# Kernel tuning notes

Hardware: AMD Instinct MI355X
Metric: run time of the kernel (lower is better)

## Reference

```python
import jax, jax.numpy as jnp
import numpy as np

N = 8192
D = 128
NUM_CLASSES = 100
EPS = 1e-8  # torch CosineSimilarity default eps


def _l2_normalize(x):
    # torch cosine sim divides by max(||x||, eps)
    n = jnp.sqrt(jnp.sum(x * x, axis=-1, keepdims=True))
    return x / jnp.maximum(n, EPS)


def _remove_diag(M):
    # [n, n] -> [n, n-1], dropping the diagonal, no boolean gather needed
    n = M.shape[0]
    return M.reshape(-1)[1:].reshape(n - 1, n + 1)[:, :-1].reshape(n, n - 1)


def setup_inputs() -> dict:
    key = jax.random.key(0)
    k1, k2, k3, k4 = jax.random.split(key, 4)
    inst_embed = jax.random.normal(k1, (N, D), dtype=jnp.float32)
    proxy = jax.random.normal(k2, (N, D), dtype=jnp.float32)
    negative_mask = jax.random.randint(k3, (NUM_CLASSES, N), 0, 2).astype(jnp.float32)
    labels = jax.random.randint(k4, (N,), 0, NUM_CLASSES, dtype=jnp.int64) if jax.config.jax_enable_x64 else jax.random.randint(k4, (N,), 0, NUM_CLASSES, dtype=jnp.int32)
    return {
        "inst_embed": inst_embed,
        "proxy": proxy,
        "negative_mask": negative_mask,
        "labels": labels,
        "temperature": jnp.float32(0.07),
        "margin": jnp.float32(0.0),
    }


def reference(inst_embed, proxy, negative_mask, labels, temperature, margin):
    xn = _l2_normalize(inst_embed)                       # [N, D]
    # pairwise cosine similarity via normalize + matmul (not NxNxD broadcast)
    sim = xn @ xn.T                                      # [N, N]
    instance_zone = jnp.exp((_remove_diag(sim) - margin) / temperature)  # [N, N-1]

    pn = _l2_normalize(proxy)
    inst2proxy_positive = jnp.exp((jnp.sum(xn * pn, axis=-1) - margin) / temperature)  # [N]

    # pos_collected_numerator == True branch
    mask = _remove_diag(negative_mask[labels])           # [N, N-1]
    numerator = jnp.sum(instance_zone * mask, axis=1) + inst2proxy_positive
    denominator = inst2proxy_positive + jnp.sum(instance_zone, axis=1)
    return -jnp.mean(jnp.log(numerator / denominator))
```

## Files before the change

### kernel.cpp

```cpp
#include <hip/hip_runtime.h>
#include <stdint.h>

#define NROWS 8192
#define DD 128
#define EPS 1e-8f
#define LOG2E 1.4426950408889634f

#define SPLIT 16
#define RPB 256
#define CPT 32
#define LDS_COL 272
#define NT ((NROWS / SPLIT) / CPT)
#define NORM_BLOCKS (NROWS / 4)
#define PACK_BLOCKS 3200

typedef __bf16 bf16x8 __attribute__((ext_vector_type(8)));
typedef float f32x4 __attribute__((ext_vector_type(4)));

__device__ __forceinline__ unsigned int f2bf(float f) {
  union { float f; unsigned int u; } v; v.f = f;
  unsigned int u = v.u;
  return (u + 0x7fffu + ((u >> 16) & 1u)) >> 16;
}
__device__ __forceinline__ float bf2f(unsigned int b) {
  union { unsigned int u; float f; } v; v.u = b << 16;
  return v.f;
}

__global__ __launch_bounds__(256) void norm_kernel(
    const float* __restrict__ x, const float* __restrict__ pr,
    const float* __restrict__ nm, const int* __restrict__ lb,
    const float* __restrict__ tptr,
    unsigned short* __restrict__ xnA, unsigned short* __restrict__ xnB,
    float* __restrict__ p, float* __restrict__ eself, float* __restrict__ mii,
    float* __restrict__ tot, float* __restrict__ msk,
    unsigned int* __restrict__ packed, float* __restrict__ out)
{
  int wave = threadIdx.x >> 6, lane = threadIdx.x & 63;
  int bx = blockIdx.x;

  if (bx >= NORM_BLOCKS) {
    int widx = (bx - NORM_BLOCKS) * 4 + wave;
    int cls = widx >> 7;
    int w64 = widx & 127;
    float v = nm[(size_t)cls * NROWS + w64 * 64 + lane];
    unsigned long long b = __ballot(v != 0.0f);
    if (lane == 0) {
      packed[cls * 256 + w64 * 2] = (unsigned int)b;
      packed[cls * 256 + w64 * 2 + 1] = (unsigned int)(b >> 32);
    }
    return;
  }

  int row = bx * 4 + wave;
  float2 xv = ((const float2*)(x + (size_t)row * DD))[lane];
  float2 pv = ((const float2*)(pr + (size_t)row * DD))[lane];
  float sx = xv.x * xv.x + xv.y * xv.y;
  float sp = pv.x * pv.x + pv.y * pv.y;
  float dp = xv.x * pv.x + xv.y * pv.y;
  #pragma unroll
  for (int m = 1; m < 64; m <<= 1) {
    sx += __shfl_xor(sx, m);
    sp += __shfl_xor(sp, m);
    dp += __shfl_xor(dp, m);
  }
  float inx = 1.f / fmaxf(sqrtf(sx), EPS);
  float inp = 1.f / fmaxf(sqrtf(sp), EPS);
  float s1 = LOG2E / tptr[0];

  unsigned int a0 = f2bf(xv.x * inx * s1), a1 = f2bf(xv.y * inx * s1);
  unsigned int b0 = f2bf(xv.x * inx),      b1 = f2bf(xv.y * inx);
  ((unsigned int*)(xnA + (size_t)row * DD))[lane] = a0 | (a1 << 16);
  ((unsigned int*)(xnB + (size_t)row * DD))[lane] = b0 | (b1 << 16);

  float ss = bf2f(a0) * bf2f(b0) + bf2f(a1) * bf2f(b1);
  #pragma unroll
  for (int m = 1; m < 64; m <<= 1) ss += __shfl_xor(ss, m);

  if (lane == 0) {
    p[row] = __builtin_amdgcn_exp2f(dp * inx * inp * s1);
    eself[row] = __builtin_amdgcn_exp2f(ss);
    mii[row] = nm[(size_t)lb[row] * NROWS + row];
    tot[row] = 0.f;
    msk[row] = 0.f;
    if (row == 0) out[0] = 0.f;
  }
}

__global__ __launch_bounds__(256, 2) void main_kernel(
    const unsigned short* __restrict__ xnA_u, const unsigned short* __restrict__ xnB_u,
    const unsigned int* __restrict__ packed, const int* __restrict__ labels,
    float* __restrict__ tot, float* __restrict__ msk)
{
  __shared__ unsigned char lds[2][CPT * LDS_COL];
  int tid = threadIdx.x;
  int wave = tid >> 6, lane = tid & 63;
  int q = lane >> 4, c = lane & 15;
  int rbase = blockIdx.x * RPB + wave * 16;

  const bf16x8* xnvA = (const bf16x8*)xnA_u;

  bf16x8 a[4][4];
  #pragma unroll
  for (int st = 0; st < 4; st++) {
    const bf16x8* b = xnvA + (size_t)(rbase + st * 64 + c) * (DD / 8) + q;
    a[st][0] = b[0]; a[st][1] = b[4]; a[st][2] = b[8]; a[st][3] = b[12];
  }

  int jb = blockIdx.y * (NROWS / SPLIT);

  unsigned int offP[4][4];
  #pragma unroll
  for (int st = 0; st < 4; st++) {
    #pragma unroll
    for (int k = 0; k < 4; k++) {
      offP[st][k] = (unsigned int)labels[rbase + st * 64 + q * 4 + k] * 256u
                  + (unsigned int)(jb >> 5);
    }
  }
  float tacc[4][4], macc[4][4];
  #pragma unroll
  for (int st = 0; st < 4; st++)
    #pragma unroll
    for (int k = 0; k < 4; k++) { tacc[st][k] = 0.f; macc[st][k] = 0.f; }

  int scol = tid >> 4, schunk = tid & 15;
  const char* gB = (const char*)xnB_u;
  const char* gbase = gB + (size_t)(jb + scol) * 256 + schunk * 16;
  unsigned int ldsoff = (unsigned int)(scol * LDS_COL + schunk * 16);

  uint4 g0 = *(const uint4*)(gbase);
  uint4 g1 = *(const uint4*)(gbase + 16 * 256);
  unsigned int wn[4][4];
  #pragma unroll
  for (int st = 0; st < 4; st++)
    #pragma unroll
    for (int k = 0; k < 4; k++) wn[st][k] = packed[offP[st][k]];
  *(uint4*)(lds[0] + ldsoff)                = g0;
  *(uint4*)(lds[0] + ldsoff + 16 * LDS_COL) = g1;
  __syncthreads();

  for (int t = 0; t < NT; t++) {
    unsigned int wc[4][4];
    #pragma unroll
    for (int st = 0; st < 4; st++)
      #pragma unroll
      for (int k = 0; k < 4; k++) wc[st][k] = wn[st][k];

    if (t + 1 < NT) {
      const char* gb = gbase + (size_t)(t + 1) * (CPT * 256);
      g0 = *(const uint4*)(gb);
      g1 = *(const uint4*)(gb + 16 * 256);
      #pragma unroll
      for (int st = 0; st < 4; st++)
        #pragma unroll
        for (int k = 0; k < 4; k++) wn[st][k] = packed[offP[st][k] + t + 1];
    }

    const unsigned char* buf = lds[t & 1];
    #pragma unroll
    for (int s = 0; s < 2; s++) {
      const bf16x8* bl = (const bf16x8*)(buf + (unsigned)(s * 16 + c) * LDS_COL + q * 16);
      bf16x8 b0 = bl[0], b1 = bl[4], b2 = bl[8], b3 = bl[12];

      f32x4 acc[4];
      #pragma unroll
      for (int st = 0; st < 4; st++) acc[st] = (f32x4){0, 0, 0, 0};
      #pragma unroll
      for (int st = 0; st < 4; st++)
        acc[st] = __builtin_amdgcn_mfma_f32_16x16x32_bf16(a[st][0], b0, acc[st], 0, 0, 0);
      #pragma unroll
      for (int st = 0; st < 4; st++)
        acc[st] = __builtin_amdgcn_mfma_f32_16x16x32_bf16(a[st][1], b1, acc[st], 0, 0, 0);
      #pragma unroll
      for (int st = 0; st < 4; st++)
        acc[st] = __builtin_amdgcn_mfma_f32_16x16x32_bf16(a[st][2], b2, acc[st], 0, 0, 0);
      #pragma unroll
      for (int st = 0; st < 4; st++)
        acc[st] = __builtin_amdgcn_mfma_f32_16x16x32_bf16(a[st][3], b3, acc[st], 0, 0, 0);

      int pos = s * 16 + c;
      #pragma unroll
      for (int st = 0; st < 4; st++) {
        #pragma unroll
        for (int k = 0; k < 4; k++) {
          float e = __builtin_amdgcn_exp2f(acc[st][k]);
          tacc[st][k] += e;
          int sm;
          asm("v_bfe_i32 %0, %1, %2, 1" : "=v"(sm) : "v"(wc[st][k]), "v"(pos));
          union { float f; int i; } u;
          u.f = e; u.i &= sm;
          macc[st][k] += u.f;
        }
      }
    }

    if (t + 1 < NT) {
      unsigned char* nb = (unsigned char*)lds[(t + 1) & 1];
      *(uint4*)(nb + ldsoff)                = g0;
      *(uint4*)(nb + ldsoff + 16 * LDS_COL) = g1;
    }
    __syncthreads();
  }

  #pragma unroll
  for (int sh = 1; sh < 16; sh <<= 1) {
    #pragma unroll
    for (int st = 0; st < 4; st++) {
      #pragma unroll
      for (int k = 0; k < 4; k++) {
        tacc[st][k] += __shfl_xor(tacc[st][k], sh);
        macc[st][k] += __shfl_xor(macc[st][k], sh);
      }
    }
  }
  if (c == 0) {
    #pragma unroll
    for (int st = 0; st < 4; st++) {
      #pragma unroll
      for (int k = 0; k < 4; k++) {
        int r = rbase + st * 64 + q * 4 + k;
        atomicAdd(&tot[r], tacc[st][k]);
        atomicAdd(&msk[r], macc[st][k]);
      }
    }
  }
}

__global__ __launch_bounds__(256) void loss_kernel(
    const float* __restrict__ p, const float* __restrict__ tot,
    const float* __restrict__ msk, const float* __restrict__ eself,
    const float* __restrict__ mii, float* __restrict__ out)
{
  __shared__ float sd[4];
  int r = blockIdx.x * 256 + threadIdx.x;
  float pi = p[r];
  float es = eself[r];
  float t = tot[r] - es;
  float m = msk[r] - es * mii[r];
  float v = __builtin_amdgcn_logf(pi + t) - __builtin_amdgcn_logf(pi + m);
  float s = v * (1.0f / (LOG2E * (float)NROWS));
  #pragma unroll
  for (int sh = 1; sh < 64; sh <<= 1) s += __shfl_xor(s, sh);
  int wave = threadIdx.x >> 6, lane = threadIdx.x & 63;
  if (lane == 0) sd[wave] = s;
  __syncthreads();
  if (threadIdx.x == 0) atomicAdd(out, sd[0] + sd[1] + sd[2] + sd[3]);
}

extern "C" void kernel_launch(void* const* d_in, const int* in_sizes, int n_in,
                              void* d_out, int out_size, void* d_ws, size_t ws_size,
                              hipStream_t stream) {
  const float* x  = (const float*)d_in[0];
  const float* pr = (const float*)d_in[1];
  const float* nm = (const float*)d_in[2];
  const int*   lb = (const int*)d_in[3];
  const float* tp = (const float*)d_in[4];

  char* ws = (char*)d_ws;
  unsigned short* xnA = (unsigned short*)ws;
  unsigned short* xnB = xnA + (size_t)NROWS * DD;
  float* p     = (float*)(xnB + (size_t)NROWS * DD);
  float* tot   = p + NROWS;
  float* msk   = tot + NROWS;
  float* eself = msk + NROWS;
  float* miiv  = eself + NROWS;
  unsigned int* packed = (unsigned int*)(miiv + NROWS);
  float* out = (float*)d_out;

  norm_kernel<<<NORM_BLOCKS + PACK_BLOCKS, 256, 0, stream>>>(
      x, pr, nm, lb, tp, xnA, xnB, p, eself, miiv, tot, msk, packed, out);
  main_kernel<<<dim3(NROWS / RPB, SPLIT), 256, 0, stream>>>(xnA, xnB, packed,
                                                            lb, tot, msk);
  loss_kernel<<<NROWS / 256, 256, 0, stream>>>(p, tot, msk, eself, miiv, out);
}
```

Before: 106.5 us.

## Exploit Gram-matrix symmetry with upper-triangular 128x128 tile pairs

Replaces the split-column streaming loop with one block per upper-triangular 128x128 tile pair. Each block computes sim once and accumulates both row sums and column sums, masking the column contribution with the transposed label mask bits. This roughly halves the MFMA and exp work. In exchange it adds a second mask extraction per element, more atomics, and drops the in-block double-buffered pipelining, since each block now holds only one tile.

```diff
diff --git a/kernel.cpp b/kernel.cpp
--- a/kernel.cpp
+++ b/kernel.cpp
@@ -6,11 +6,10 @@
 #define EPS 1e-8f
 #define LOG2E 1.4426950408889634f
 
-#define SPLIT 16
-#define RPB 256
-#define CPT 32
+#define TB 128
+#define NTILE (NROWS / TB)
+#define NPAIRS (NTILE * (NTILE + 1) / 2)
 #define LDS_COL 272
-#define NT ((NROWS / SPLIT) / CPT)
 #define NORM_BLOCKS (NROWS / 4)
 #define PACK_BLOCKS 3200
 
@@ -92,115 +91,115 @@
     const unsigned int* __restrict__ packed, const int* __restrict__ labels,
     float* __restrict__ tot, float* __restrict__ msk)
 {
-  __shared__ unsigned char lds[2][CPT * LDS_COL];
+  __shared__ unsigned char lds[TB * LDS_COL];
   int tid = threadIdx.x;
   int wave = tid >> 6, lane = tid & 63;
   int q = lane >> 4, c = lane & 15;
-  int rbase = blockIdx.x * RPB + wave * 16;
+  int wm = wave >> 1, wn = wave & 1;
+
+  int bid = blockIdx.x;
+  int ri = (int)((129.0f - sqrtf(129.0f * 129.0f - 8.0f * (float)bid)) * 0.5f);
+  while (ri * (129 - ri) / 2 > bid) ri--;
+  while ((ri + 1) * (128 - ri) / 2 <= bid) ri++;
+  int cj = ri + (bid - ri * (129 - ri) / 2);
+  int rblock = ri * TB, colbase = cj * TB;
+
+  int scol = tid & 127, sh8 = (tid >> 7) * 8;
+  const uint4* gsrc = (const uint4*)((const char*)xnB_u + (size_t)(colbase + scol) * 256) + sh8;
+  uint4 stg[8];
+  #pragma unroll
+  for (int u = 0; u < 8; u++) stg[u] = gsrc[u];
 
   const bf16x8* xnvA = (const bf16x8*)xnA_u;
-
   bf16x8 a[4][4];
   #pragma unroll
   for (int st = 0; st < 4; st++) {
-    const bf16x8* b = xnvA + (size_t)(rbase + st * 64 + c) * (DD / 8) + q;
-    a[st][0] = b[0]; a[st][1] = b[4]; a[st][2] = b[8]; a[st][3] = b[12];
-  }
-
-  int jb = blockIdx.y * (NROWS / SPLIT);
-
-  unsigned int offP[4][4];
+    const bf16x8* ap = xnvA + (size_t)(rblock + wm * 64 + st * 16 + c) * (DD / 8) + q;
+    a[st][0] = ap[0]; a[st][1] = ap[4]; a[st][2] = ap[8]; a[st][3] = ap[12];
+  }
+
+  int q4 = q * 4;
+  int cw0 = (colbase >> 5) + wn * 2;
+  unsigned wrow[2][4][4];
   #pragma unroll
   for (int st = 0; st < 4; st++) {
     #pragma unroll
     for (int k = 0; k < 4; k++) {
-      offP[st][k] = (unsigned int)labels[rbase + st * 64 + q * 4 + k] * 256u
-                  + (unsigned int)(jb >> 5);
-    }
-  }
-  float tacc[4][4], macc[4][4];
+      unsigned off = (unsigned)labels[rblock + wm * 64 + st * 16 + q4 + k] * 256u + cw0;
+      wrow[0][st][k] = packed[off];
+      wrow[1][st][k] = packed[off + 1];
+    }
+  }
+  int rw0 = (rblock >> 5) + wm * 2;
+  unsigned cwv[4][2];
+  #pragma unroll
+  for (int g = 0; g < 4; g++) {
+    unsigned off = (unsigned)labels[colbase + wn * 64 + g * 16 + c] * 256u + rw0;
+    cwv[g][0] = packed[off];
+    cwv[g][1] = packed[off + 1];
+  }
+
+  {
+    uint4* dst = (uint4*)(lds + (unsigned)(scol * LDS_COL) + sh8 * 16);
+    #pragma unroll
+    for (int u = 0; u < 8; u++) dst[u] = stg[u];
+  }
+  __syncthreads();
+
+  float tacc[4][4], macc[4][4], tcol[4], mcol[4];
   #pragma unroll
   for (int st = 0; st < 4; st++)
     #pragma unroll
     for (int k = 0; k < 4; k++) { tacc[st][k] = 0.f; macc[st][k] = 0.f; }
-
-  int scol = tid >> 4, schunk = tid & 15;
-  const char* gB = (const char*)xnB_u;
-  const char* gbase = gB + (size_t)(jb + scol) * 256 + schunk * 16;
-  unsigned int ldsoff = (unsigned int)(scol * LDS_COL + schunk * 16);
-
-  uint4 g0 = *(const uint4*)(gbase);
-  uint4 g1 = *(const uint4*)(gbase + 16 * 256);
-  unsigned int wn[4][4];
-  #pragma unroll
-  for (int st = 0; st < 4; st++)
-    #pragma unroll
-    for (int k = 0; k < 4; k++) wn[st][k] = packed[offP[st][k]];
-  *(uint4*)(lds[0] + ldsoff)                = g0;
-  *(uint4*)(lds[0] + ldsoff + 16 * LDS_COL) = g1;
-  __syncthreads();
-
-  for (int t = 0; t < NT; t++) {
-    unsigned int wc[4][4];
-    #pragma unroll
-    for (int st = 0; st < 4; st++)
+  #pragma unroll
+  for (int g = 0; g < 4; g++) { tcol[g] = 0.f; mcol[g] = 0.f; }
+
+  int posr0 = c, posr1 = c + 16;
+
+  #pragma unroll
+  for (int g = 0; g < 4; g++) {
+    const bf16x8* bl = (const bf16x8*)(lds + (unsigned)((wn * 64 + g * 16 + c) * LDS_COL) + q * 16);
+    bf16x8 b0 = bl[0], b1 = bl[4], b2 = bl[8], b3 = bl[12];
+
+    f32x4 acc[4];
+    #pragma unroll
+    for (int st = 0; st < 4; st++) acc[st] = (f32x4){0, 0, 0, 0};
+    #pragma unroll
+    for (int st = 0; st < 4; st++)
+      acc[st] = __builtin_amdgcn_mfma_f32_16x16x32_bf16(a[st][0], b0, acc[st], 0, 0, 0);
+    #pragma unroll
+    for (int st = 0; st < 4; st++)
+      acc[st] = __builtin_amdgcn_mfma_f32_16x16x32_bf16(a[st][1], b1, acc[st], 0, 0, 0);
+    #pragma unroll
+    for (int st = 0; st < 4; st++)
+      acc[st] = __builtin_amdgcn_mfma_f32_16x16x32_bf16(a[st][2], b2, acc[st], 0, 0, 0);
+    #pragma unroll
+    for (int st = 0; st < 4; st++)
+      acc[st] = __builtin_amdgcn_mfma_f32_16x16x32_bf16(a[st][3], b3, acc[st], 0, 0, 0);
+
+    unsigned cwqA = cwv[g][0] >> q4;
+    unsigned cwqB = cwv[g][1] >> q4;
+    int posr = (g & 1) ? posr1 : posr0;
+
+    #pragma unroll
+    for (int st = 0; st < 4; st++) {
+      unsigned cwq = (st < 2) ? cwqA : cwqB;
       #pragma unroll
-      for (int k = 0; k < 4; k++) wc[st][k] = wn[st][k];
-
-    if (t + 1 < NT) {
-      const char* gb = gbase + (size_t)(t + 1) * (CPT * 256);
-      g0 = *(const uint4*)(gb);
-      g1 = *(const uint4*)(gb + 16 * 256);
-      #pragma unroll
-      for (int st = 0; st < 4; st++)
-        #pragma unroll
-        for (int k = 0; k < 4; k++) wn[st][k] = packed[offP[st][k] + t + 1];
-    }
-
-    const unsigned char* buf = lds[t & 1];
-    #pragma unroll
-    for (int s = 0; s < 2; s++) {
-      const bf16x8* bl = (const bf16x8*)(buf + (unsigned)(s * 16 + c) * LDS_COL + q * 16);
-      bf16x8 b0 = bl[0], b1 = bl[4], b2 = bl[8], b3 = bl[12];
-
-      f32x4 acc[4];
-      #pragma unroll
-      for (int st = 0; st < 4; st++) acc[st] = (f32x4){0, 0, 0, 0};
-      #pragma unroll
-      for (int st = 0; st < 4; st++)
-        acc[st] = __builtin_amdgcn_mfma_f32_16x16x32_bf16(a[st][0], b0, acc[st], 0, 0, 0);
-      #pragma unroll
-      for (int st = 0; st < 4; st++)
-        acc[st] = __builtin_amdgcn_mfma_f32_16x16x32_bf16(a[st][1], b1, acc[st], 0, 0, 0);
-      #pragma unroll
-      for (int st = 0; st < 4; st++)
-        acc[st] = __builtin_amdgcn_mfma_f32_16x16x32_bf16(a[st][2], b2, acc[st], 0, 0, 0);
-      #pragma unroll
-      for (int st = 0; st < 4; st++)
-        acc[st] = __builtin_amdgcn_mfma_f32_16x16x32_bf16(a[st][3], b3, acc[st], 0, 0, 0);
-
-      int pos = s * 16 + c;
-      #pragma unroll
-      for (int st = 0; st < 4; st++) {
-        #pragma unroll
-        for (int k = 0; k < 4; k++) {
-          float e = __builtin_amdgcn_exp2f(acc[st][k]);
-          tacc[st][k] += e;
-          int sm;
-          asm("v_bfe_i32 %0, %1, %2, 1" : "=v"(sm) : "v"(wc[st][k]), "v"(pos));
-          union { float f; int i; } u;
-          u.f = e; u.i &= sm;
-          macc[st][k] += u.f;
-        }
+      for (int k = 0; k < 4; k++) {
+        float e = __builtin_amdgcn_exp2f(acc[st][k]);
+        tacc[st][k] += e;
+        int smr;
+        asm("v_bfe_i32 %0, %1, %2, 1" : "=v"(smr) : "v"(wrow[g >> 1][st][k]), "v"(posr));
+        union { float f; int i; } ur; ur.f = e; ur.i &= smr;
+        macc[st][k] += ur.f;
+        tcol[g] += e;
+        int posc = (st & 1) * 16 + k;
+        int smc;
+        asm("v_bfe_i32 %0, %1, %2, 1" : "=v"(smc) : "v"(cwq), "v"(posc));
+        union { float f; int i; } uc; uc.f = e; uc.i &= smc;
+        mcol[g] += uc.f;
       }
     }
-
-    if (t + 1 < NT) {
-      unsigned char* nb = (unsigned char*)lds[(t + 1) & 1];
-      *(uint4*)(nb + ldsoff)                = g0;
-      *(uint4*)(nb + ldsoff + 16 * LDS_COL) = g1;
-    }
-    __syncthreads();
   }
 
   #pragma unroll
@@ -219,10 +218,24 @@
     for (int st = 0; st < 4; st++) {
       #pragma unroll
       for (int k = 0; k < 4; k++) {
-        int r = rbase + st * 64 + q * 4 + k;
+        int r = rblock + wm * 64 + st * 16 + q4 + k;
         atomicAdd(&tot[r], tacc[st][k]);
         atomicAdd(&msk[r], macc[st][k]);
       }
+    }
+  }
+
+  #pragma unroll
+  for (int g = 0; g < 4; g++) {
+    tcol[g] += __shfl_xor(tcol[g], 16); tcol[g] += __shfl_xor(tcol[g], 32);
+    mcol[g] += __shfl_xor(mcol[g], 16); mcol[g] += __shfl_xor(mcol[g], 32);
+  }
+  if (ri != cj && q == 0) {
+    #pragma unroll
+    for (int g = 0; g < 4; g++) {
+      int j = colbase + wn * 64 + g * 16 + c;
+      atomicAdd(&tot[j], tcol[g]);
+      atomicAdd(&msk[j], mcol[g]);
     }
   }
 }
@@ -270,7 +283,6 @@
 
   norm_kernel<<<NORM_BLOCKS + PACK_BLOCKS, 256, 0, stream>>>(
       x, pr, nm, lb, tp, xnA, xnB, p, eself, miiv, tot, msk, packed, out);
-  main_kernel<<<dim3(NROWS / RPB, SPLIT), 256, 0, stream>>>(xnA, xnB, packed,
-                                                            lb, tot, msk);
+  main_kernel<<<NPAIRS, 256, 0, stream>>>(xnA, xnB, packed, lb, tot, msk);
   loss_kernel<<<NROWS / 256, 256, 0, stream>>>(p, tot, msk, eself, miiv, out);
 }
```

Result: slower. 155.1 us (+45.5%).
